# Kernel optimization log

Hardware: AMD Instinct MI355X
Metric: run time of the kernel (lower is better)

Reference implementation:

```python
import jax, jax.numpy as jnp
import numpy as np

B, D, H, C, P, HP = 65536, 256, 512, 10, 10, 128


def setup_inputs() -> dict:
    key = jax.random.key(0)
    ks = jax.random.split(key, 6)
    return {
        "x": jax.random.normal(ks[0], (B, D), jnp.float32),
        "Wt1": jax.random.normal(ks[1], (D, H), jnp.float32) * (1.0 / np.sqrt(D)),
        "bt1": jnp.zeros((H,), jnp.float32),
        "Wt2": jax.random.normal(ks[2], (H, C), jnp.float32) * (1.0 / np.sqrt(H)),
        "bt2": jnp.zeros((C,), jnp.float32),
        "Wp1": jax.random.normal(ks[3], (P, D, HP), jnp.float32) * (1.0 / np.sqrt(D)),
        "bp1": jnp.zeros((P, HP), jnp.float32),
        "Wp2": jax.random.normal(ks[4], (P, HP, C), jnp.float32) * (1.0 / np.sqrt(HP)),
        "bp2": jnp.zeros((P, C), jnp.float32),
        "repair_direction_dict": jax.random.randint(ks[5], (P, 2), 0, C, jnp.int32),
    }


def _get_bitmap(out, rdd):
    # torch.topk(out, 2): indices of the two largest logits per row
    _, idx = jax.lax.top_k(out, 2)                                  # [B, 2]
    # is_in[b, p] = all(idx[b] == rdd[p])  (exact top-2 pair match)
    is_in = jnp.all(idx[:, None, :] == rdd[None, :, :], axis=-1)     # [B, P]
    no_match = ~jnp.any(is_in, axis=-1)                              # [B]
    # fallback for unmatched rows: top-1 index equals rdd[:, 0]
    fallback = idx[:, :1] == rdd[None, :, 0]                         # [B, P]
    return jnp.where(no_match[:, None], fallback, is_in)             # bool [B, P]


def reference(x, Wt1, bt1, Wt2, bt2, Wp1, bp1, Wp2, bp2, repair_direction_dict):
    # target net forward: out = target_net(x)
    out = jnp.maximum(x @ Wt1 + bt1, 0.0) @ Wt2 + bt2                # [B, C]
    # bitmap computed under no_grad in the original -> stop_gradient
    bitmap = jax.lax.stop_gradient(
        _get_bitmap(out, repair_direction_dict)
    ).astype(out.dtype)                                              # [B, P]
    # each patch net runs on the FULL batch (as in the original), then the
    # bitmap gates the scatter-add combine: out[bits] += p_out[bits]
    h = jnp.maximum(jnp.einsum('bd,pdh->pbh', x, Wp1) + bp1[:, None, :], 0.0)  # [P, B, HP]
    p_out = jnp.einsum('pbh,phc->pbc', h, Wp2) + bp2[:, None, :]     # [P, B, C]
    return out + jnp.einsum('bp,pbc->bc', bitmap, p_out)             # [B, C]
```

## Files before the change

kernel.cpp:

```cpp
#include <hip/hip_runtime.h>

typedef unsigned int u32;
typedef unsigned short u16;
typedef _Float16 f16;
typedef __attribute__((ext_vector_type(8))) _Float16 f16x8;
typedef __attribute__((ext_vector_type(4))) float f32x4;

#define MARGIN 1e-2f
#define LSC 2048.0f
#define LSCI (1.0f/2048.0f)

__device__ __forceinline__ u16 f16b(float f) {
    return __builtin_bit_cast(u16, (f16)f);
}
__device__ __forceinline__ f32x4 MF(f16x8 a, f16x8 b, f32x4 c) {
    return __builtin_amdgcn_mfma_f32_16x16x32_f16(a, b, c, 0, 0, 0);
}
__device__ __forceinline__ uint4 pack8(const u16 v[8]) {
    uint4 pk;
    pk.x = (u32)v[0] | ((u32)v[1] << 16);
    pk.y = (u32)v[2] | ((u32)v[3] << 16);
    pk.z = (u32)v[4] | ((u32)v[5] << 16);
    pk.w = (u32)v[6] | ((u32)v[7] << 16);
    return pk;
}

__global__ __launch_bounds__(256) void conv_kernel(
    const float* __restrict__ Wt1, const float* __restrict__ Wp1,
    const float* __restrict__ Wt2, const float* __restrict__ Wp2,
    u16* __restrict__ wt1f, u16* __restrict__ wt1g, u16* __restrict__ wp1f,
    u16* __restrict__ wt2f, u16* __restrict__ wt2g, u16* __restrict__ wp2f,
    u32* __restrict__ gcnt)
{
    __shared__ float tile[64][68];
    const int t = threadIdx.x;
    const int b = blockIdx.x;

    if (b == 112) {
        if (t == 0) gcnt[0] = 0;
        for (int cc = t; cc < 1024; cc += 256) {
            int kk = cc >> 6, l = cc & 63, ln = l & 15, quad = l >> 4;
            u16 vh[8], vl[8];
            #pragma unroll
            for (int j = 0; j < 8; ++j) {
                int k = kk * 32 + quad * 8 + j;
                float f = (ln < 10) ? Wt2[k * 10 + ln] : 0.f;
                f16 h = (f16)f;
                vh[j] = __builtin_bit_cast(u16, h);
                vl[j] = f16b(LSC * (f - (float)h));
            }
            *(uint4*)(wt2f + kk * 512 + l * 8) = pack8(vh);
            *(uint4*)(wt2g + kk * 512 + l * 8) = pack8(vl);
        }
        for (int cc = t; cc < 2560; cc += 256) {
            int p = cc >> 8, rem = cc & 255, kk = rem >> 6, l = rem & 63;
            int ln = l & 15, quad = (l >> 4) & 3;
            u16 v[8];
            #pragma unroll
            for (int j = 0; j < 8; ++j) {
                int k = kk * 32 + quad * 8 + j;
                v[j] = f16b(ln < 10 ? Wp2[p * 1280 + k * 10 + ln] : 0.f);
            }
            *(uint4*)(wp2f + p * 2048 + kk * 512 + l * 8) = pack8(v);
        }
        return;
    }

    const float* src; int src_ld;
    u16 *dsth, *dstl; int nf0, kk0;
    if (b < 32) {
        int kt = b & 3, nt = b >> 2;
        src = Wt1 + (size_t)(kt * 64) * 512 + nt * 64; src_ld = 512;
        dsth = wt1f; dstl = wt1g; nf0 = nt * 4; kk0 = kt * 2;
    } else {
        int j = b - 32, p = j >> 3, r = j & 7;
        int kt = r & 3, nt = r >> 2;
        src = Wp1 + (size_t)p * 32768 + (size_t)(kt * 64) * 128 + nt * 64; src_ld = 128;
        dsth = wp1f + p * 32768; dstl = nullptr; nf0 = nt * 4; kk0 = kt * 2;
    }
    {
        const int kr = t >> 2, c0 = (t & 3) * 16;
        #pragma unroll
        for (int u = 0; u < 4; ++u) {
            float4 v = *(const float4*)(src + (size_t)kr * src_ld + c0 + u * 4);
            tile[kr][c0 + u*4 + 0] = v.x;
            tile[kr][c0 + u*4 + 1] = v.y;
            tile[kr][c0 + u*4 + 2] = v.z;
            tile[kr][c0 + u*4 + 3] = v.w;
        }
    }
    __syncthreads();
    #pragma unroll
    for (int s = 0; s < 2; ++s) {
        int cc = t + 256 * s;
        int l = cc & 63, fp = cc >> 6, nfl = fp >> 1, kkl = fp & 1;
        int ln = l & 15, quad = (l >> 4) & 3;
        int nloc = nfl * 16 + ln, kloc = kkl * 32 + quad * 8;
        u16 vh[8], vl[8];
        #pragma unroll
        for (int j = 0; j < 8; ++j) {
            float f = tile[kloc + j][nloc];
            f16 h = (f16)f;
            vh[j] = __builtin_bit_cast(u16, h);
            vl[j] = f16b(LSC * (f - (float)h));
        }
        size_t off = (size_t)((nf0 + nfl) * 8 + (kk0 + kkl)) * 512 + l * 8;
        *(uint4*)(dsth + off) = pack8(vh);
        if (dstl) *(uint4*)(dstl + off) = pack8(vl);
    }
}

#define LDT(Q,K2) (*(const f16x8*)(wt2f + (size_t)((Q)*4+(K2))*512 + lane*8))
#define L1G(BR, NF, KK) \
    acc[0][NF]=MF(a0,BR,acc[0][NF]); acc[1][NF]=MF(a1,BR,acc[1][NF]); \
    acc[2][NF]=MF(a2,BR,acc[2][NF]); acc[3][NF]=MF(a3,BR,acc[3][NF]); \
    if ((KK)<7) BR = *(const f16x8*)(wb1 + ((NF)*8+(KK)+1)*512);

__global__ __launch_bounds__(512, 4) void netsum_kernel(
    const float* __restrict__ x, const float* __restrict__ bt1,
    const float* __restrict__ bt2,
    const float* __restrict__ bp1, const float* __restrict__ bp2,
    const int* __restrict__ rdd,
    const u16* __restrict__ wt1f, const u16* __restrict__ wp1f,
    const u16* __restrict__ wt2f, const u16* __restrict__ wp2f,
    float* __restrict__ out, u32* __restrict__ gcnt, u32* __restrict__ glist)
{
    __shared__ u16 xf[64][264];
    __shared__ u16 scratch[17920];
    __shared__ float lg[64][10];
    __shared__ float oacc[64][10];
    __shared__ u32 plist[10][64];
    __shared__ u32 pcnt[10];
    __shared__ int rdds[20];
    __shared__ u32 wq[40];
    __shared__ u32 nwork;

    const int t = threadIdx.x;
    const int lane = t & 63;
    const int w = t >> 6;
    const int ln = lane & 15;
    const int quad = lane >> 4;
    const int row0 = blockIdx.x * 64;

    if (t < 10) pcnt[t] = 0;
    if (t < 20) rdds[t] = rdd[t];
    if (t == 0) nwork = 0;
    for (int i = t; i < 640; i += 512) ((float*)oacc)[i] = 0.f;

    #pragma unroll
    for (int i = 0; i < 8; ++i) {
        int f = t + 512 * i;
        int r = f >> 6, c4 = f & 63;
        float4 v = *(const float4*)(x + (size_t)(row0 + r) * 256 + c4 * 4);
        u16 q0 = f16b(v.x), q1 = f16b(v.y), q2 = f16b(v.z), q3 = f16b(v.w);
        uint2 pw = { (u32)q0 | ((u32)q1 << 16), (u32)q2 | ((u32)q3 << 16) };
        *(uint2*)&xf[r][c4 * 4] = pw;
    }
    const u16* wb1 = wt1f + (size_t)(w * 32) * 512 + (size_t)lane * 8;
    f16x8 bA = *(const f16x8*)(wb1 + 0 * 512);
    f16x8 bB = *(const f16x8*)(wb1 + 8 * 512);
    f16x8 bC = *(const f16x8*)(wb1 + 16 * 512);
    f16x8 bD = *(const f16x8*)(wb1 + 24 * 512);
    f16x8 t0 = {}, t1 = {}, t2 = {}, t3 = {};
    if (w < 4) { t0 = LDT(0,0); t1 = LDT(0,1); t2 = LDT(0,2); t3 = LDT(0,3); }
    __syncthreads();

    f32x4 acc[4][4];
    #pragma unroll
    for (int m = 0; m < 4; ++m)
        #pragma unroll
        for (int i2 = 0; i2 < 4; ++i2) acc[m][i2] = (f32x4){0.f,0.f,0.f,0.f};
    #pragma unroll
    for (int kk = 0; kk < 8; ++kk) {
        f16x8 a0 = *(const f16x8*)(&xf[ 0 + ln][kk*32 + quad*8]);
        f16x8 a1 = *(const f16x8*)(&xf[16 + ln][kk*32 + quad*8]);
        f16x8 a2 = *(const f16x8*)(&xf[32 + ln][kk*32 + quad*8]);
        f16x8 a3 = *(const f16x8*)(&xf[48 + ln][kk*32 + quad*8]);
        L1G(bA, 0, kk)
        L1G(bB, 1, kk)
        L1G(bC, 2, kk)
        L1G(bD, 3, kk)
    }

    f32x4 acc2 = (f32x4){0.f, 0.f, 0.f, 0.f};
    u16* hq = scratch;
    for (int q = 0; q < 4; ++q) {
        if ((w >> 1) == q) {
            const int nfl0 = (w & 1) * 4;
            #pragma unroll
            for (int i2 = 0; i2 < 4; ++i2) {
                const int colL = (nfl0 + i2) * 16 + ln;
                const float bias = bt1[q * 128 + colL];
                #pragma unroll
                for (int m = 0; m < 4; ++m)
                    #pragma unroll
                    for (int r = 0; r < 4; ++r) {
                        float hv = acc[m][i2][r] + bias; hv = hv > 0.f ? hv : 0.f;
                        hq[(m * 16 + quad * 4 + r) * 140 + colL] = f16b(hv);
                    }
            }
        }
        __syncthreads();
        if (w < 4) {
            acc2 = MF(*(const f16x8*)(&hq[(w*16+ln)*140 + 0*32 + quad*8]), t0, acc2);
            acc2 = MF(*(const f16x8*)(&hq[(w*16+ln)*140 + 1*32 + quad*8]), t1, acc2);
            acc2 = MF(*(const f16x8*)(&hq[(w*16+ln)*140 + 2*32 + quad*8]), t2, acc2);
            acc2 = MF(*(const f16x8*)(&hq[(w*16+ln)*140 + 3*32 + quad*8]), t3, acc2);
            if (q < 3) { t0 = LDT(q+1,0); t1 = LDT(q+1,1); t2 = LDT(q+1,2); t3 = LDT(q+1,3); }
        }
        __syncthreads();
    }
    if (w < 4 && ln < 10) {
        #pragma unroll
        for (int r = 0; r < 4; ++r)
            lg[w * 16 + quad * 4 + r][ln] = acc2[r] + bt2[ln];
    }
    __syncthreads();

    if (t < 64) {
        float l[10];
        #pragma unroll
        for (int c = 0; c < 10; ++c) l[c] = lg[t][c];
        float b0v = -1e30f; int i0 = 0;
        #pragma unroll
        for (int c = 0; c < 10; ++c) if (l[c] > b0v) { b0v = l[c]; i0 = c; }
        float b1v = -1e30f; int i1 = 0;
        #pragma unroll
        for (int c = 0; c < 10; ++c) { if (c == i0) continue; if (l[c] > b1v) { b1v = l[c]; i1 = c; } }
        float b2v = -1e30f;
        #pragma unroll
        for (int c = 0; c < 10; ++c) { if (c == i0 || c == i1) continue; if (l[c] > b2v) b2v = l[c]; }
        if (b0v - b1v < MARGIN || b1v - b2v < MARGIN) {
            u32 idx = atomicAdd(gcnt, 1u);
            glist[idx] = (u32)(row0 + t);
        }
        u32 exact = 0, fb = 0;
        #pragma unroll
        for (int p = 0; p < 10; ++p) {
            int a = rdds[2 * p], bq = rdds[2 * p + 1];
            if (i0 == a && i1 == bq) exact |= 1u << p;
            if (i0 == a)             fb    |= 1u << p;
        }
        u32 bits = exact ? exact : fb;
        while (bits) {
            int p = __ffs(bits) - 1;
            bits &= bits - 1;
            u32 idx = atomicAdd(&pcnt[p], 1u);
            plist[p][idx] = (u32)t;
        }
    }
    __syncthreads();
    if (t < 10) {
        int L = (int)pcnt[t];
        for (int base = 0; base < L; base += 16) {
            u32 e = atomicAdd(&nwork, 1u);
            wq[e] = ((u32)t << 8) | (u32)base;
        }
    }
    __syncthreads();

    {
        const u32 nw = nwork;
        for (u32 ii = w; ii < nw; ii += 8) {
            const u32 item = wq[ii];
            const int p = (int)(item >> 8), mbase = (int)(item & 255);
            const int Lp = (int)pcnt[p];
            const int mi = mbase + ln;
            const int arow = (mi < Lp) ? (int)plist[p][mi] : (int)plist[p][0];
            const u16* xr = &xf[arow][0];
            const u16* wb = wp1f + (size_t)p * 32768 + (size_t)lane * 8;
            u16* hp = &scratch[w * 2240];
            #pragma unroll
            for (int g = 0; g < 2; ++g) {
                f32x4 acc4[4];
                #pragma unroll
                for (int i2 = 0; i2 < 4; ++i2) acc4[i2] = (f32x4){0.f,0.f,0.f,0.f};
                f16x8 wc4[4];
                #pragma unroll
                for (int i2 = 0; i2 < 4; ++i2)
                    wc4[i2] = *(const f16x8*)(wb + ((g * 4 + i2) * 8 + 0) * 512);
                #pragma unroll
                for (int kk = 0; kk < 8; ++kk) {
                    f16x8 wn4[4];
                    #pragma unroll
                    for (int i2 = 0; i2 < 4; ++i2) {
                        wn4[i2] = wc4[i2];
                        if (kk < 7)
                            wn4[i2] = *(const f16x8*)(wb + ((g * 4 + i2) * 8 + kk + 1) * 512);
                    }
                    f16x8 a = *(const f16x8*)(xr + kk * 32 + quad * 8);
                    #pragma unroll
                    for (int i2 = 0; i2 < 4; ++i2) acc4[i2] = MF(a, wc4[i2], acc4[i2]);
                    #pragma unroll
                    for (int i2 = 0; i2 < 4; ++i2) wc4[i2] = wn4[i2];
                }
                #pragma unroll
                for (int i2 = 0; i2 < 4; ++i2) {
                    const int i2g = g * 4 + i2;
                    float bias = bp1[p * 128 + i2g * 16 + ln];
                    #pragma unroll
                    for (int r = 0; r < 4; ++r) {
                        float hv = acc4[i2][r] + bias; hv = hv > 0.f ? hv : 0.f;
                        hp[(quad * 4 + r) * 140 + i2g * 16 + ln] = f16b(hv);
                    }
                }
            }
            f32x4 po = (f32x4){0.f,0.f,0.f,0.f};
            #pragma unroll
            for (int kk = 0; kk < 4; ++kk) {
                f16x8 ha = *(const f16x8*)(&hp[ln * 140 + kk * 32 + quad * 8]);
                f16x8 wb2 = *(const f16x8*)(wp2f + p * 2048 + kk * 512 + lane * 8);
                po = MF(ha, wb2, po);
            }
            if (ln < 10) {
                float b2 = bp2[p * 10 + ln];
                #pragma unroll
                for (int r = 0; r < 4; ++r) {
                    int mi2 = mbase + quad * 4 + r;
                    if (mi2 < Lp)
                        atomicAdd(&oacc[plist[p][mi2]][ln], po[r] + b2);
                }
            }
        }
    }
    __syncthreads();

    for (int i = t; i < 640; i += 512)
        out[(size_t)row0 * 10 + i] = ((float*)lg)[i] + ((float*)oacc)[i];
}

#define FLD(S,KK) \
    S##h0 = *(const f16x8*)(bbh + (KK)*512); \
    S##h1 = *(const f16x8*)(bbh + 4096 + (KK)*512); \
    S##l0 = *(const f16x8*)(bbl + (KK)*512); \
    S##l1 = *(const f16x8*)(bbl + 4096 + (KK)*512);
#define FCP(S,KK) { _Pragma("unroll") for (int m_=0;m_<4;++m_){ \
    f16x8 ah_=*(const f16x8*)(&xfh[m_*16+ln][(KK)*32+quad*8]); \
    f16x8 al_=*(const f16x8*)(&xfl[m_*16+ln][(KK)*32+quad*8]); \
    accH[m_][0]=MF(ah_,S##h0,accH[m_][0]); accS[m_][0]=MF(ah_,S##l0,accS[m_][0]); accS[m_][0]=MF(al_,S##h0,accS[m_][0]); \
    accH[m_][1]=MF(ah_,S##h1,accH[m_][1]); accS[m_][1]=MF(ah_,S##l1,accS[m_][1]); accS[m_][1]=MF(al_,S##h1,accS[m_][1]); } }
#define F2L(WH, WL, KK) \
    WH = *(const f16x8*)(wt2f + (hl*8+(KK))*512 + lane*8); \
    WL = *(const f16x8*)(wt2g + (hl*8+(KK))*512 + lane*8);
#define F2C(WH, WL, KK) { int hidx_=(w*16+ln)*264 + (KK)*32 + quad*8; \
    f16x8 hah_=*(const f16x8*)(&hb2[0][hidx_]); f16x8 hal_=*(const f16x8*)(&hb2[1][hidx_]); \
    acc2h=MF(hah_,WH,acc2h); acc2s=MF(hah_,WL,acc2s); acc2s=MF(hal_,WH,acc2s); }

__global__ __launch_bounds__(512, 1) void fix_kernel(
    const float* __restrict__ x, const float* __restrict__ bt1,
    const float* __restrict__ bt2,
    const float* __restrict__ bp1, const float* __restrict__ bp2,
    const int* __restrict__ rdd,
    const u16* __restrict__ wt1f, const u16* __restrict__ wt1g,
    const u16* __restrict__ wt2f, const u16* __restrict__ wt2g,
    const u16* __restrict__ wp1f, const u16* __restrict__ wp2f,
    const u32* __restrict__ gcnt, const u32* __restrict__ glist,
    float* __restrict__ out)
{
    __shared__ u16 xfh[64][264];
    __shared__ u16 xfl[64][264];
    __shared__ u16 hb2[2][16896];
    __shared__ float lg[64][10];
    __shared__ float oacc[64][10];
    __shared__ u32 rows[64];
    __shared__ u32 plist[10][64];
    __shared__ u32 pcnt[10];
    __shared__ int rdds[20];
    __shared__ u32 wq[40];
    __shared__ u32 nwork;

    const int t = threadIdx.x;
    const int lane = t & 63;
    const int w = t >> 6;
    const int ln = lane & 15;
    const int quad = lane >> 4;
    const u32 cnt = gcnt[0];
    if (t < 20) rdds[t] = rdd[t];

    for (u32 base = blockIdx.x * 64; base < cnt; base += gridDim.x * 64) {
        __syncthreads();
        const int R = (int)min(64u, cnt - base);
        if (t < 64) rows[t] = glist[base + (t < R ? t : 0)];
        if (t < 10) pcnt[t] = 0;
        if (t == 0) nwork = 0;
        for (int i = t; i < 640; i += 512) ((float*)oacc)[i] = 0.f;
        __syncthreads();

        #pragma unroll
        for (int i = 0; i < 8; ++i) {
            int f = t + 512 * i;
            int r = f >> 6, c4 = f & 63;
            float4 v = *(const float4*)(x + (size_t)rows[r] * 256 + c4 * 4);
            f16 h0 = (f16)v.x, h1 = (f16)v.y, h2 = (f16)v.z, h3 = (f16)v.w;
            u16 q0 = __builtin_bit_cast(u16, h0), q1 = __builtin_bit_cast(u16, h1);
            u16 q2 = __builtin_bit_cast(u16, h2), q3 = __builtin_bit_cast(u16, h3);
            u16 l0 = f16b(LSC * (v.x - (float)h0)), l1 = f16b(LSC * (v.y - (float)h1));
            u16 l2 = f16b(LSC * (v.z - (float)h2)), l3 = f16b(LSC * (v.w - (float)h3));
            uint2 hw = { (u32)q0 | ((u32)q1 << 16), (u32)q2 | ((u32)q3 << 16) };
            uint2 lw = { (u32)l0 | ((u32)l1 << 16), (u32)l2 | ((u32)l3 << 16) };
            *(uint2*)&xfh[r][c4 * 4] = hw;
            *(uint2*)&xfl[r][c4 * 4] = lw;
        }
        __syncthreads();

        f32x4 acc2h = (f32x4){0.f,0.f,0.f,0.f};
        f32x4 acc2s = (f32x4){0.f,0.f,0.f,0.f};
        for (int hl = 0; hl < 2; ++hl) {
            f32x4 accH[4][2], accS[4][2];
            #pragma unroll
            for (int m = 0; m < 4; ++m)
                #pragma unroll
                for (int i2 = 0; i2 < 2; ++i2) {
                    accH[m][i2] = (f32x4){0.f,0.f,0.f,0.f};
                    accS[m][i2] = (f32x4){0.f,0.f,0.f,0.f};
                }
            const size_t boff = (size_t)(hl * 16 + w * 2) * 4096 + (size_t)lane * 8;
            const u16* bbh = wt1f + boff;
            const u16* bbl = wt1g + boff;
            f16x8 ch0, ch1, cl0, cl1, nh0, nh1, nl0, nl1;
            FLD(c,0);
            FLD(n,1); FCP(c,0);
            FLD(c,2); FCP(n,1);
            FLD(n,3); FCP(c,2);
            FLD(c,4); FCP(n,3);
            FLD(n,5); FCP(c,4);
            FLD(c,6); FCP(n,5);
            FLD(n,7); FCP(c,6);
            FCP(n,7);
            #pragma unroll
            for (int m = 0; m < 4; ++m)
                #pragma unroll
                for (int i2 = 0; i2 < 2; ++i2) {
                    int nloc = w * 32 + i2 * 16 + ln;
                    float bias = bt1[hl * 256 + nloc];
                    #pragma unroll
                    for (int r = 0; r < 4; ++r) {
                        float hv = accH[m][i2][r] + accS[m][i2][r] * LSCI + bias;
                        hv = hv > 0.f ? hv : 0.f;
                        f16 hh = (f16)hv;
                        int idx = (m * 16 + quad * 4 + r) * 264 + nloc;
                        hb2[0][idx] = __builtin_bit_cast(u16, hh);
                        hb2[1][idx] = f16b(LSC * (hv - (float)hh));
                    }
                }
            __syncthreads();
            if (w < 4) {
                f16x8 whc, wlc, whn, wln;
                F2L(whc, wlc, 0);
                F2L(whn, wln, 1); F2C(whc, wlc, 0);
                F2L(whc, wlc, 2); F2C(whn, wln, 1);
                F2L(whn, wln, 3); F2C(whc, wlc, 2);
                F2L(whc, wlc, 4); F2C(whn, wln, 3);
                F2L(whn, wln, 5); F2C(whc, wlc, 4);
                F2L(whc, wlc, 6); F2C(whn, wln, 5);
                F2L(whn, wln, 7); F2C(whc, wlc, 6);
                F2C(whn, wln, 7);
            }
            __syncthreads();
        }
        if (w < 4 && ln < 10) {
            #pragma unroll
            for (int r = 0; r < 4; ++r)
                lg[w * 16 + quad * 4 + r][ln] = acc2h[r] + acc2s[r] * LSCI + bt2[ln];
        }
        __syncthreads();

        if (t < R) {
            float l[10];
            #pragma unroll
            for (int c = 0; c < 10; ++c) l[c] = lg[t][c];
            float b0v = -1e30f; int i0 = 0;
            #pragma unroll
            for (int c = 0; c < 10; ++c) if (l[c] > b0v) { b0v = l[c]; i0 = c; }
            float b1v = -1e30f; int i1 = 0;
            #pragma unroll
            for (int c = 0; c < 10; ++c) { if (c == i0) continue; if (l[c] > b1v) { b1v = l[c]; i1 = c; } }
            u32 exact = 0, fb = 0;
            #pragma unroll
            for (int p = 0; p < 10; ++p) {
                int a = rdds[2 * p], bq = rdds[2 * p + 1];
                if (i0 == a && i1 == bq) exact |= 1u << p;
                if (i0 == a)             fb    |= 1u << p;
            }
            u32 bits = exact ? exact : fb;
            while (bits) {
                int p = __ffs(bits) - 1;
                bits &= bits - 1;
                u32 idx = atomicAdd(&pcnt[p], 1u);
                plist[p][idx] = (u32)t;
            }
        }
        __syncthreads();
        if (t < 10) {
            int L = (int)pcnt[t];
            for (int b2i = 0; b2i < L; b2i += 16) {
                u32 e = atomicAdd(&nwork, 1u);
                wq[e] = ((u32)t << 8) | (u32)b2i;
            }
        }
        __syncthreads();

        {
            const u32 nw = nwork;
            u16* hbase = &hb2[0][0];
            for (u32 ii = w; ii < nw; ii += 8) {
                const u32 item = wq[ii];
                const int p = (int)(item >> 8), mbase = (int)(item & 255);
                const int Lp = (int)pcnt[p];
                const int mi = mbase + ln;
                const int arow = (mi < Lp) ? (int)plist[p][mi] : (int)plist[p][0];
                const u16* xr = &xfh[arow][0];
                const u16* wb = wp1f + (size_t)p * 32768 + (size_t)lane * 8;
                u16* hp = hbase + w * 2176;
                #pragma unroll
                for (int g = 0; g < 2; ++g) {
                    f32x4 acc4[4];
                    #pragma unroll
                    for (int i2 = 0; i2 < 4; ++i2) acc4[i2] = (f32x4){0.f,0.f,0.f,0.f};
                    f16x8 wc4[4];
                    #pragma unroll
                    for (int i2 = 0; i2 < 4; ++i2)
                        wc4[i2] = *(const f16x8*)(wb + ((g * 4 + i2) * 8 + 0) * 512);
                    #pragma unroll
                    for (int kk = 0; kk < 8; ++kk) {
                        f16x8 wn4[4];
                        #pragma unroll
                        for (int i2 = 0; i2 < 4; ++i2) {
                            wn4[i2] = wc4[i2];
                            if (kk < 7)
                                wn4[i2] = *(const f16x8*)(wb + ((g * 4 + i2) * 8 + kk + 1) * 512);
                        }
                        f16x8 a = *(const f16x8*)(xr + kk * 32 + quad * 8);
                        #pragma unroll
                        for (int i2 = 0; i2 < 4; ++i2) acc4[i2] = MF(a, wc4[i2], acc4[i2]);
                        #pragma unroll
                        for (int i2 = 0; i2 < 4; ++i2) wc4[i2] = wn4[i2];
                    }
                    #pragma unroll
                    for (int i2 = 0; i2 < 4; ++i2) {
                        const int i2g = g * 4 + i2;
                        float bias = bp1[p * 128 + i2g * 16 + ln];
                        #pragma unroll
                        for (int r = 0; r < 4; ++r) {
                            float hv = acc4[i2][r] + bias; hv = hv > 0.f ? hv : 0.f;
                            hp[(quad * 4 + r) * 136 + i2g * 16 + ln] = f16b(hv);
                        }
                    }
                }
                f32x4 po = (f32x4){0.f,0.f,0.f,0.f};
                #pragma unroll
                for (int kk = 0; kk < 4; ++kk) {
                    f16x8 ha = *(const f16x8*)(&hp[ln * 136 + kk * 32 + quad * 8]);
                    f16x8 wb2 = *(const f16x8*)(wp2f + p * 2048 + kk * 512 + lane * 8);
                    po = MF(ha, wb2, po);
                }
                if (ln < 10) {
                    float b2 = bp2[p * 10 + ln];
                    #pragma unroll
                    for (int r = 0; r < 4; ++r) {
                        int mi2 = mbase + quad * 4 + r;
                        if (mi2 < Lp)
                            atomicAdd(&oacc[plist[p][mi2]][ln], po[r] + b2);
                    }
                }
            }
        }
        __syncthreads();

        for (int i = t; i < R * 10; i += 512) {
            int r = i / 10, c = i % 10;
            out[(size_t)rows[r] * 10 + c] = lg[r][c] + oacc[r][c];
        }
    }
}

extern "C" void kernel_launch(void* const* d_in, const int* in_sizes, int n_in,
                              void* d_out, int out_size, void* d_ws, size_t ws_size,
                              hipStream_t stream) {
    const float* x   = (const float*)d_in[0];
    const float* Wt1 = (const float*)d_in[1];
    const float* bt1 = (const float*)d_in[2];
    const float* Wt2 = (const float*)d_in[3];
    const float* bt2 = (const float*)d_in[4];
    const float* Wp1 = (const float*)d_in[5];
    const float* bp1 = (const float*)d_in[6];
    const float* Wp2 = (const float*)d_in[7];
    const float* bp2 = (const float*)d_in[8];
    const int* rdd = (const int*)d_in[9];
    float* out = (float*)d_out;

    u16* wt1f = (u16*)d_ws;
    u16* wt1g = wt1f + 131072;
    u16* wp1f = wt1g + 131072;
    u16* wt2f = wp1f + 327680;
    u16* wt2g = wt2f + 8192;
    u16* wp2f = wt2g + 8192;
    u32* gcnt  = (u32*)(wp2f + 20480);
    u32* glist = gcnt + 16;

    hipLaunchKernelGGL(conv_kernel, dim3(113), dim3(256), 0, stream,
                       Wt1, Wp1, Wt2, Wp2, wt1f, wt1g, wp1f, wt2f, wt2g, wp2f, gcnt);
    hipLaunchKernelGGL(netsum_kernel, dim3(1024), dim3(512), 0, stream,
                       x, bt1, bt2, bp1, bp2, rdd,
                       wt1f, wp1f, wt2f, wp2f, out, gcnt, glist);
    hipLaunchKernelGGL(fix_kernel, dim3(256), dim3(512), 0, stream,
                       x, bt1, bt2, bp1, bp2, rdd,
                       wt1f, wt1g, wt2f, wt2g, wp1f, wp2f,
                       gcnt, glist, out);
}
```

Baseline: 214.6 us.

## Restructure layer-1 GEMM per quarter and skip fixup rows whose top-2 is unchanged

```diff
diff --git a/kernel.cpp b/kernel.cpp
--- a/kernel.cpp
+++ b/kernel.cpp
@@ -110,12 +110,6 @@
     }
 }
 
-#define LDT(Q,K2) (*(const f16x8*)(wt2f + (size_t)((Q)*4+(K2))*512 + lane*8))
-#define L1G(BR, NF, KK) \
-    acc[0][NF]=MF(a0,BR,acc[0][NF]); acc[1][NF]=MF(a1,BR,acc[1][NF]); \
-    acc[2][NF]=MF(a2,BR,acc[2][NF]); acc[3][NF]=MF(a3,BR,acc[3][NF]); \
-    if ((KK)<7) BR = *(const f16x8*)(wb1 + ((NF)*8+(KK)+1)*512);
-
 __global__ __launch_bounds__(512, 4) void netsum_kernel(
     const float* __restrict__ x, const float* __restrict__ bt1,
     const float* __restrict__ bt2,
@@ -126,7 +120,7 @@
     float* __restrict__ out, u32* __restrict__ gcnt, u32* __restrict__ glist)
 {
     __shared__ u16 xf[64][264];
-    __shared__ u16 scratch[17920];
+    __shared__ u16 scratch[17408];
     __shared__ float lg[64][10];
     __shared__ float oacc[64][10];
     __shared__ u32 plist[10][64];
@@ -156,57 +150,46 @@
         uint2 pw = { (u32)q0 | ((u32)q1 << 16), (u32)q2 | ((u32)q3 << 16) };
         *(uint2*)&xf[r][c4 * 4] = pw;
     }
-    const u16* wb1 = wt1f + (size_t)(w * 32) * 512 + (size_t)lane * 8;
-    f16x8 bA = *(const f16x8*)(wb1 + 0 * 512);
-    f16x8 bB = *(const f16x8*)(wb1 + 8 * 512);
-    f16x8 bC = *(const f16x8*)(wb1 + 16 * 512);
-    f16x8 bD = *(const f16x8*)(wb1 + 24 * 512);
-    f16x8 t0 = {}, t1 = {}, t2 = {}, t3 = {};
-    if (w < 4) { t0 = LDT(0,0); t1 = LDT(0,1); t2 = LDT(0,2); t3 = LDT(0,3); }
     __syncthreads();
-
-    f32x4 acc[4][4];
-    #pragma unroll
-    for (int m = 0; m < 4; ++m)
-        #pragma unroll
-        for (int i2 = 0; i2 < 4; ++i2) acc[m][i2] = (f32x4){0.f,0.f,0.f,0.f};
-    #pragma unroll
-    for (int kk = 0; kk < 8; ++kk) {
-        f16x8 a0 = *(const f16x8*)(&xf[ 0 + ln][kk*32 + quad*8]);
-        f16x8 a1 = *(const f16x8*)(&xf[16 + ln][kk*32 + quad*8]);
-        f16x8 a2 = *(const f16x8*)(&xf[32 + ln][kk*32 + quad*8]);
-        f16x8 a3 = *(const f16x8*)(&xf[48 + ln][kk*32 + quad*8]);
-        L1G(bA, 0, kk)
-        L1G(bB, 1, kk)
-        L1G(bC, 2, kk)
-        L1G(bD, 3, kk)
-    }
 
     f32x4 acc2 = (f32x4){0.f, 0.f, 0.f, 0.f};
     u16* hq = scratch;
     for (int q = 0; q < 4; ++q) {
-        if ((w >> 1) == q) {
-            const int nfl0 = (w & 1) * 4;
-            #pragma unroll
-            for (int i2 = 0; i2 < 4; ++i2) {
-                const int colL = (nfl0 + i2) * 16 + ln;
-                const float bias = bt1[q * 128 + colL];
-                #pragma unroll
-                for (int m = 0; m < 4; ++m)
-                    #pragma unroll
-                    for (int r = 0; r < 4; ++r) {
-                        float hv = acc[m][i2][r] + bias; hv = hv > 0.f ? hv : 0.f;
-                        hq[(m * 16 + quad * 4 + r) * 140 + colL] = f16b(hv);
-                    }
-            }
+        f32x4 acc[4];
+        #pragma unroll
+        for (int m = 0; m < 4; ++m) acc[m] = (f32x4){0.f,0.f,0.f,0.f};
+        const u16* bb = wt1f + (size_t)((q * 8 + w) * 8) * 512 + (size_t)lane * 8;
+        f16x8 wc = *(const f16x8*)bb;
+        #pragma unroll
+        for (int kk = 0; kk < 8; ++kk) {
+            f16x8 wn = wc;
+            if (kk < 7) wn = *(const f16x8*)(bb + (kk + 1) * 512);
+            #pragma unroll
+            for (int m = 0; m < 4; ++m) {
+                f16x8 a = *(const f16x8*)(&xf[m * 16 + ln][kk * 32 + quad * 8]);
+                acc[m] = MF(a, wc, acc[m]);
+            }
+            wc = wn;
+        }
+        {
+            const int nloc = w * 16 + ln;
+            const float bias = bt1[q * 128 + nloc];
+            #pragma unroll
+            for (int m = 0; m < 4; ++m)
+                #pragma unroll
+                for (int r = 0; r < 4; ++r) {
+                    float hv = acc[m][r] + bias; hv = hv > 0.f ? hv : 0.f;
+                    hq[(m * 16 + quad * 4 + r) * 136 + nloc] = f16b(hv);
+                }
         }
         __syncthreads();
         if (w < 4) {
-            acc2 = MF(*(const f16x8*)(&hq[(w*16+ln)*140 + 0*32 + quad*8]), t0, acc2);
-            acc2 = MF(*(const f16x8*)(&hq[(w*16+ln)*140 + 1*32 + quad*8]), t1, acc2);
-            acc2 = MF(*(const f16x8*)(&hq[(w*16+ln)*140 + 2*32 + quad*8]), t2, acc2);
-            acc2 = MF(*(const f16x8*)(&hq[(w*16+ln)*140 + 3*32 + quad*8]), t3, acc2);
-            if (q < 3) { t0 = LDT(q+1,0); t1 = LDT(q+1,1); t2 = LDT(q+1,2); t3 = LDT(q+1,3); }
+            #pragma unroll
+            for (int kk2 = 0; kk2 < 4; ++kk2) {
+                f16x8 ha = *(const f16x8*)(&hq[(w * 16 + ln) * 136 + kk2 * 32 + quad * 8]);
+                f16x8 wb = *(const f16x8*)(wt2f + (q * 4 + kk2) * 512 + lane * 8);
+                acc2 = MF(ha, wb, acc2);
+            }
         }
         __syncthreads();
     }
@@ -232,7 +215,7 @@
         for (int c = 0; c < 10; ++c) { if (c == i0 || c == i1) continue; if (l[c] > b2v) b2v = l[c]; }
         if (b0v - b1v < MARGIN || b1v - b2v < MARGIN) {
             u32 idx = atomicAdd(gcnt, 1u);
-            glist[idx] = (u32)(row0 + t);
+            glist[idx] = (u32)(row0 + t) | ((u32)i0 << 16) | ((u32)i1 << 20);
         }
         u32 exact = 0, fb = 0;
         #pragma unroll
@@ -269,7 +252,7 @@
             const int arow = (mi < Lp) ? (int)plist[p][mi] : (int)plist[p][0];
             const u16* xr = &xf[arow][0];
             const u16* wb = wp1f + (size_t)p * 32768 + (size_t)lane * 8;
-            u16* hp = &scratch[w * 2240];
+            u16* hp = &scratch[w * 2176];
             #pragma unroll
             for (int g = 0; g < 2; ++g) {
                 f32x4 acc4[4];
@@ -301,14 +284,14 @@
                     #pragma unroll
                     for (int r = 0; r < 4; ++r) {
                         float hv = acc4[i2][r] + bias; hv = hv > 0.f ? hv : 0.f;
-                        hp[(quad * 4 + r) * 140 + i2g * 16 + ln] = f16b(hv);
+                        hp[(quad * 4 + r) * 136 + i2g * 16 + ln] = f16b(hv);
                     }
                 }
             }
             f32x4 po = (f32x4){0.f,0.f,0.f,0.f};
             #pragma unroll
             for (int kk = 0; kk < 4; ++kk) {
-                f16x8 ha = *(const f16x8*)(&hp[ln * 140 + kk * 32 + quad * 8]);
+                f16x8 ha = *(const f16x8*)(&hp[ln * 136 + kk * 32 + quad * 8]);
                 f16x8 wb2 = *(const f16x8*)(wp2f + p * 2048 + kk * 512 + lane * 8);
                 po = MF(ha, wb2, po);
             }
@@ -363,6 +346,8 @@
     __shared__ float lg[64][10];
     __shared__ float oacc[64][10];
     __shared__ u32 rows[64];
+    __shared__ u32 nspair[64];
+    __shared__ u32 chg[64];
     __shared__ u32 plist[10][64];
     __shared__ u32 pcnt[10];
     __shared__ int rdds[20];
@@ -380,7 +365,12 @@
     for (u32 base = blockIdx.x * 64; base < cnt; base += gridDim.x * 64) {
         __syncthreads();
         const int R = (int)min(64u, cnt - base);
-        if (t < 64) rows[t] = glist[base + (t < R ? t : 0)];
+        if (t < 64) {
+            u32 g = glist[base + (t < R ? t : 0)];
+            rows[t] = g & 0xFFFFu;
+            nspair[t] = (g >> 16) & 0xFFu;
+            chg[t] = 0;
+        }
         if (t < 10) pcnt[t] = 0;
         if (t == 0) nwork = 0;
         for (int i = t; i < 640; i += 512) ((float*)oacc)[i] = 0.f;
@@ -475,19 +465,23 @@
             float b1v = -1e30f; int i1 = 0;
             #pragma unroll
             for (int c = 0; c < 10; ++c) { if (c == i0) continue; if (l[c] > b1v) { b1v = l[c]; i1 = c; } }
-            u32 exact = 0, fb = 0;
-            #pragma unroll
-            for (int p = 0; p < 10; ++p) {
-                int a = rdds[2 * p], bq = rdds[2 * p + 1];
-                if (i0 == a && i1 == bq) exact |= 1u << p;
-                if (i0 == a)             fb    |= 1u << p;
-            }
-            u32 bits = exact ? exact : fb;
-            while (bits) {
-                int p = __ffs(bits) - 1;
-                bits &= bits - 1;
-                u32 idx = atomicAdd(&pcnt[p], 1u);
-                plist[p][idx] = (u32)t;
+            u32 ep = (u32)i0 | ((u32)i1 << 4);
+            if (ep != nspair[t]) {
+                chg[t] = 1;
+                u32 exact = 0, fb = 0;
+                #pragma unroll
+                for (int p = 0; p < 10; ++p) {
+                    int a = rdds[2 * p], bq = rdds[2 * p + 1];
+                    if (i0 == a && i1 == bq) exact |= 1u << p;
+                    if (i0 == a)             fb    |= 1u << p;
+                }
+                u32 bits = exact ? exact : fb;
+                while (bits) {
+                    int p = __ffs(bits) - 1;
+                    bits &= bits - 1;
+                    u32 idx = atomicAdd(&pcnt[p], 1u);
+                    plist[p][idx] = (u32)t;
+                }
             }
         }
         __syncthreads();
@@ -569,7 +563,8 @@
 
         for (int i = t; i < R * 10; i += 512) {
             int r = i / 10, c = i % 10;
-            out[(size_t)rows[r] * 10 + c] = lg[r][c] + oacc[r][c];
+            if (chg[r])
+                out[(size_t)rows[r] * 10 + c] = lg[r][c] + oacc[r][c];
         }
     }
 }
```

After: 193.3 us. -9.9%, faster.
